# Performance work log

Measured on AMD Instinct MI355X. Metric: run time of the kernel, lower is better.

## Reference

```python
import jax, jax.numpy as jnp
import numpy as np

WINDOW_SIZE = 5
CONSISTENCY_WEIGHT = 1.0


def _wsum(x, w):
    # sliding-window sum along axis 1 via exclusive cumsum differences
    s = jnp.cumsum(x, axis=1)
    s = jnp.pad(s, ((0, 0), (1, 0)))
    return s[:, w:] - s[:, :-w]  # [B, L-w+1]


def setup_inputs() -> dict:
    key = jax.random.key(0)
    k1, k2, k3 = jax.random.split(key, 3)
    B, L, C = 512, 16384, 2
    return {
        "predictions": jax.random.normal(k1, (B, L, C), dtype=jnp.float32),
        "targets": jax.random.randint(k2, (B, L), 0, 2, dtype=jnp.int32),
        "mask": jax.random.randint(k3, (B, L), 0, 2, dtype=jnp.int32),
    }


def reference(predictions, targets, mask):
    w = WINDOW_SIZE
    probs = jax.nn.softmax(predictions, axis=-1)[..., 1]  # [B, L]
    t = targets.astype(jnp.float32)
    m = mask.astype(jnp.float32)

    msum = _wsum(m, w)                       # [B, W]
    denom = jnp.maximum(msum, 1.0)           # clamp(min=1.0)
    spm = _wsum(probs * m, w)
    stm = _wsum(t * m, w)
    sp2m = _wsum(probs * probs * m, w)
    st2m = _wsum(t * t * m, w)

    pmean = spm / denom
    tmean = stm / denom
    # masked biased variance: sum((x - mean)^2 * m) / clamp(msum, 1)
    pvar = (sp2m - 2.0 * pmean * spm + pmean * pmean * msum) / denom
    tvar = (st2m - 2.0 * tmean * stm + tmean * tmean * msum) / denom

    mse = jnp.mean((pvar - tvar) ** 2, axis=0)          # per-window MSE over batch, [W]
    valid = (jnp.sum(msum, axis=0) > 0).astype(jnp.float32)  # skip windows with zero mask
    cnt = jnp.maximum(jnp.sum(valid), 1.0)
    loss = jnp.sum(mse * valid) / cnt * CONSISTENCY_WEIGHT
    return loss
```

## Files before the change

### kernel.cpp

```cpp
#include <hip/hip_runtime.h>
#include <math.h>

#define BATCH 512
#define LEN   16384
#define WIN   5
#define WOUT  (LEN - WIN + 1)

__global__ void bcl_partial_kernel(const float* __restrict__ pred,
                                   const int*   __restrict__ tgt,
                                   const int*   __restrict__ msk,
                                   float* __restrict__ part_d2,
                                   float* __restrict__ part_ms,
                                   int bper) {
    int j = blockIdx.x * blockDim.x + threadIdx.x;
    if (j >= WOUT) return;
    int b0 = blockIdx.y * bper;
    float accd2 = 0.f, accms = 0.f;
    for (int b = b0; b < b0 + bper; ++b) {
        const float2* pr = (const float2*)(pred + ((size_t)b * LEN + j) * 2);
        const int*    tb = tgt + (size_t)b * LEN + j;
        const int*    mb = msk + (size_t)b * LEN + j;
        float msum = 0.f, spm = 0.f, stm = 0.f, sp2m = 0.f;
#pragma unroll
        for (int k = 0; k < WIN; ++k) {
            float  m  = (float)mb[k];
            float  t  = (float)tb[k];
            float2 p2 = pr[k];
            float  p  = 1.0f / (1.0f + __expf(p2.x - p2.y));
            msum += m;
            spm  += p * m;
            stm  += t * m;
            sp2m += p * p * m;
        }
        float denom = fmaxf(msum, 1.0f);
        float pmean = spm / denom;
        float tmean = stm / denom;
        float pvar  = (sp2m - 2.0f * pmean * spm + pmean * pmean * msum) / denom;
        float tvar  = (stm  - 2.0f * tmean * stm + tmean * tmean * msum) / denom;
        float d = pvar - tvar;
        accd2 += d * d;
        accms += msum;
    }
    part_d2[(size_t)blockIdx.y * WOUT + j] = accd2;
    part_ms[(size_t)blockIdx.y * WOUT + j] = accms;
}

__global__ void bcl_window_reduce(const float* __restrict__ part_d2,
                                  const float* __restrict__ part_ms,
                                  double* __restrict__ blk_out,
                                  int nchunks) {
    int j = blockIdx.x * blockDim.x + threadIdx.x;
    double num = 0.0, cnt = 0.0;
    if (j < WOUT) {
        float d2 = 0.f, ms = 0.f;
        for (int c = 0; c < nchunks; ++c) {
            d2 += part_d2[(size_t)c * WOUT + j];
            ms += part_ms[(size_t)c * WOUT + j];
        }
        if (ms > 0.f) {
            num = (double)d2 * (1.0 / (double)BATCH);
            cnt = 1.0;
        }
    }
    for (int off = 32; off > 0; off >>= 1) {
        num += __shfl_down(num, off, 64);
        cnt += __shfl_down(cnt, off, 64);
    }
    __shared__ double s_num[8], s_cnt[8];
    int lane = threadIdx.x & 63, wave = threadIdx.x >> 6;
    if (lane == 0) { s_num[wave] = num; s_cnt[wave] = cnt; }
    __syncthreads();
    if (threadIdx.x == 0) {
        double n = 0.0, c = 0.0;
        int nw = (int)(blockDim.x >> 6);
        for (int wv = 0; wv < nw; ++wv) { n += s_num[wv]; c += s_cnt[wv]; }
        blk_out[(size_t)blockIdx.x * 2]     = n;
        blk_out[(size_t)blockIdx.x * 2 + 1] = c;
    }
}

__global__ void bcl_final(const double* __restrict__ blk_out,
                          float* __restrict__ out, int nblk) {
    double num = 0.0, cnt = 0.0;
    for (int i = threadIdx.x; i < nblk; i += 64) {
        num += blk_out[(size_t)i * 2];
        cnt += blk_out[(size_t)i * 2 + 1];
    }
    for (int off = 32; off > 0; off >>= 1) {
        num += __shfl_down(num, off, 64);
        cnt += __shfl_down(cnt, off, 64);
    }
    if (threadIdx.x == 0) out[0] = (float)(num / fmax(cnt, 1.0));
}

extern "C" void kernel_launch(void* const* d_in, const int* in_sizes, int n_in,
                              void* d_out, int out_size, void* d_ws, size_t ws_size,
                              hipStream_t stream) {
    const float* pred = (const float*)d_in[0];
    const int*   tgt  = (const int*)d_in[1];
    const int*   msk  = (const int*)d_in[2];
    float* out = (float*)d_out;

    int nchunks = 16;
    while (nchunks > 1) {
        size_t need = (size_t)nchunks * WOUT * 2 * sizeof(float) + 64 * 2 * sizeof(double) + 64;
        if (need <= ws_size) break;
        nchunks >>= 1;
    }
    int bper = BATCH / nchunks;

    float* part_d2 = (float*)d_ws;
    float* part_ms = part_d2 + (size_t)nchunks * WOUT;
    size_t off = ((size_t)nchunks * WOUT * 2 * sizeof(float) + 7) & ~(size_t)7;
    double* blk_out = (double*)((char*)d_ws + off);

    const int TPB = 256;
    const int WBLKS = (WOUT + TPB - 1) / TPB;

    dim3 g1(WBLKS, nchunks);
    bcl_partial_kernel<<<g1, TPB, 0, stream>>>(pred, tgt, msk, part_d2, part_ms, bper);

    bcl_window_reduce<<<WBLKS, TPB, 0, stream>>>(part_d2, part_ms, blk_out, nchunks);

    bcl_final<<<1, 64, 0, stream>>>(blk_out, out, WBLKS);
}
```

Baseline: 168.7 us.

## Stage per-element window inputs in shared memory and fuse final reduction via atomics

The partial kernel now loads each element once per tile into shared memory, computing the sigmoid and masked products a single time instead of five times per element across overlapping windows. The window sums then read from LDS. The separate final kernel is replaced by double atomics plus a ticket counter in the window-reduce kernel, and the chunk count is raised from 16 to 32. This adds two __syncthreads per batch row and a memset launch, and the atomic reduction order is nondeterministic.

```diff
diff --git a/kernel.cpp b/kernel.cpp
--- a/kernel.cpp
+++ b/kernel.cpp
@@ -5,6 +5,9 @@
 #define LEN   16384
 #define WIN   5
 #define WOUT  (LEN - WIN + 1)
+#define TPB   256
+#define TILE  256
+#define ELEMS (TILE + WIN - 1)
 
 __global__ void bcl_partial_kernel(const float* __restrict__ pred,
                                    const int*   __restrict__ tgt,
@@ -12,44 +15,68 @@
                                    float* __restrict__ part_d2,
                                    float* __restrict__ part_ms,
                                    int bper) {
-    int j = blockIdx.x * blockDim.x + threadIdx.x;
-    if (j >= WOUT) return;
-    int b0 = blockIdx.y * bper;
+    __shared__ float s_m[ELEMS], s_tm[ELEMS], s_pm[ELEMS], s_p2m[ELEMS];
+
+    const int tile0 = blockIdx.x * TILE;
+    const int j     = tile0 + threadIdx.x;
+    const int b0    = blockIdx.y * bper;
+
     float accd2 = 0.f, accms = 0.f;
+
     for (int b = b0; b < b0 + bper; ++b) {
-        const float2* pr = (const float2*)(pred + ((size_t)b * LEN + j) * 2);
-        const int*    tb = tgt + (size_t)b * LEN + j;
-        const int*    mb = msk + (size_t)b * LEN + j;
-        float msum = 0.f, spm = 0.f, stm = 0.f, sp2m = 0.f;
+        __syncthreads();
+        for (int i = threadIdx.x; i < ELEMS; i += TPB) {
+            const int e = tile0 + i;
+            float m = 0.f, tmf = 0.f, p = 0.f;
+            if (e < LEN) {
+                const size_t base = (size_t)b * LEN + e;
+                const int    mi = msk[base];
+                const int    ti = tgt[base];
+                const float2 p2 = ((const float2*)pred)[base];
+                p   = 1.0f / (1.0f + __expf(p2.x - p2.y));
+                m   = (float)mi;
+                tmf = (float)(ti & mi);
+            }
+            s_m[i]   = m;
+            s_tm[i]  = tmf;
+            s_pm[i]  = p * m;
+            s_p2m[i] = p * p * m;
+        }
+        __syncthreads();
+        if (j < WOUT) {
+            float msum = 0.f, stm = 0.f, spm = 0.f, sp2m = 0.f;
 #pragma unroll
-        for (int k = 0; k < WIN; ++k) {
-            float  m  = (float)mb[k];
-            float  t  = (float)tb[k];
-            float2 p2 = pr[k];
-            float  p  = 1.0f / (1.0f + __expf(p2.x - p2.y));
-            msum += m;
-            spm  += p * m;
-            stm  += t * m;
-            sp2m += p * p * m;
+            for (int k = 0; k < WIN; ++k) {
+                const int i = threadIdx.x + k;
+                msum += s_m[i];
+                stm  += s_tm[i];
+                spm  += s_pm[i];
+                sp2m += s_p2m[i];
+            }
+            const float denom = fmaxf(msum, 1.0f);
+            const float inv   = 1.0f / denom;
+            const float pmean = spm * inv;
+            const float tmean = stm * inv;
+            const float pvar  = (sp2m - 2.0f * pmean * spm + pmean * pmean * msum) * inv;
+            const float tvar  = (stm  - 2.0f * tmean * stm + tmean * tmean * msum) * inv;
+            const float d = pvar - tvar;
+            accd2 += d * d;
+            accms += msum;
         }
-        float denom = fmaxf(msum, 1.0f);
-        float pmean = spm / denom;
-        float tmean = stm / denom;
-        float pvar  = (sp2m - 2.0f * pmean * spm + pmean * pmean * msum) / denom;
-        float tvar  = (stm  - 2.0f * tmean * stm + tmean * tmean * msum) / denom;
-        float d = pvar - tvar;
-        accd2 += d * d;
-        accms += msum;
     }
-    part_d2[(size_t)blockIdx.y * WOUT + j] = accd2;
-    part_ms[(size_t)blockIdx.y * WOUT + j] = accms;
+    if (j < WOUT) {
+        part_d2[(size_t)blockIdx.y * WOUT + j] = accd2;
+        part_ms[(size_t)blockIdx.y * WOUT + j] = accms;
+    }
 }
 
 __global__ void bcl_window_reduce(const float* __restrict__ part_d2,
                                   const float* __restrict__ part_ms,
-                                  double* __restrict__ blk_out,
+                                  double* __restrict__ accum,
+                                  unsigned int* __restrict__ ticket,
+                                  float* __restrict__ out,
                                   int nchunks) {
-    int j = blockIdx.x * blockDim.x + threadIdx.x;
+    const int j = blockIdx.x * blockDim.x + threadIdx.x;
     double num = 0.0, cnt = 0.0;
     if (j < WOUT) {
         float d2 = 0.f, ms = 0.f;
@@ -66,31 +93,22 @@
         num += __shfl_down(num, off, 64);
         cnt += __shfl_down(cnt, off, 64);
     }
-    __shared__ double s_num[8], s_cnt[8];
-    int lane = threadIdx.x & 63, wave = threadIdx.x >> 6;
+    __shared__ double s_num[4], s_cnt[4];
+    const int lane = threadIdx.x & 63, wave = threadIdx.x >> 6;
     if (lane == 0) { s_num[wave] = num; s_cnt[wave] = cnt; }
     __syncthreads();
     if (threadIdx.x == 0) {
         double n = 0.0, c = 0.0;
-        int nw = (int)(blockDim.x >> 6);
+        const int nw = (int)(blockDim.x >> 6);
         for (int wv = 0; wv < nw; ++wv) { n += s_num[wv]; c += s_cnt[wv]; }
-        blk_out[(size_t)blockIdx.x * 2]     = n;
-        blk_out[(size_t)blockIdx.x * 2 + 1] = c;
+        atomicAdd(&accum[0], n);
+        atomicAdd(&accum[1], c);
+        __threadfence();
+        const unsigned int t = atomicAdd(ticket, 1u);
+        if (t == gridDim.x - 1) {
+            out[0] = (float)(accum[0] / fmax(accum[1], 1.0));
+        }
     }
-}
-
-__global__ void bcl_final(const double* __restrict__ blk_out,
-                          float* __restrict__ out, int nblk) {
-    double num = 0.0, cnt = 0.0;
-    for (int i = threadIdx.x; i < nblk; i += 64) {
-        num += blk_out[(size_t)i * 2];
-        cnt += blk_out[(size_t)i * 2 + 1];
-    }
-    for (int off = 32; off > 0; off >>= 1) {
-        num += __shfl_down(num, off, 64);
-        cnt += __shfl_down(cnt, off, 64);
-    }
-    if (threadIdx.x == 0) out[0] = (float)(num / fmax(cnt, 1.0));
 }
 
 extern "C" void kernel_launch(void* const* d_in, const int* in_sizes, int n_in,
@@ -101,26 +119,26 @@
     const int*   msk  = (const int*)d_in[2];
     float* out = (float*)d_out;
 
-    int nchunks = 16;
+    int nchunks = 32;
     while (nchunks > 1) {
-        size_t need = (size_t)nchunks * WOUT * 2 * sizeof(float) + 64 * 2 * sizeof(double) + 64;
+        size_t need = (size_t)nchunks * WOUT * 2 * sizeof(float) + 64;
         if (need <= ws_size) break;
         nchunks >>= 1;
     }
-    int bper = BATCH / nchunks;
+    const int bper = BATCH / nchunks;
 
     float* part_d2 = (float*)d_ws;
     float* part_ms = part_d2 + (size_t)nchunks * WOUT;
-    size_t off = ((size_t)nchunks * WOUT * 2 * sizeof(float) + 7) & ~(size_t)7;
-    double* blk_out = (double*)((char*)d_ws + off);
+    size_t off = ((size_t)nchunks * WOUT * 2 * sizeof(float) + 15) & ~(size_t)15;
+    double* accum = (double*)((char*)d_ws + off);
+    unsigned int* ticket = (unsigned int*)(accum + 2);
 
-    const int TPB = 256;
-    const int WBLKS = (WOUT + TPB - 1) / TPB;
+    hipMemsetAsync((void*)accum, 0, 2 * sizeof(double) + sizeof(unsigned int), stream);
+
+    const int WBLKS = (WOUT + TILE - 1) / TILE;
 
     dim3 g1(WBLKS, nchunks);
     bcl_partial_kernel<<<g1, TPB, 0, stream>>>(pred, tgt, msk, part_d2, part_ms, bper);
 
-    bcl_window_reduce<<<WBLKS, TPB, 0, stream>>>(part_d2, part_ms, blk_out, nchunks);
-
-    bcl_final<<<1, 64, 0, stream>>>(blk_out, out, WBLKS);
+    bcl_window_reduce<<<WBLKS, TPB, 0, stream>>>(part_d2, part_ms, accum, ticket, out, nchunks);
 }
```

New measurement: 167.9 us. About the same (-0.5%).
